# Performance work log

Measured on AMD Instinct MI355X. Metric: run time of the kernel, lower is better.

## Reference

```python
import jax, jax.numpy as jnp
import numpy as np

N, E, C, R = 10000, 160000, 128, 8
D = 4 * C  # 128x0e + 128x1o -> 128*1 + 128*3
INV_SQRT3 = float(1.0 / np.sqrt(3.0))  # CG norm for 1x1->0
INV_SQRT2 = float(1.0 / np.sqrt(2.0))  # CG norm for 1x1->1 (cross)
LIN_SCALE = float(1.0 / np.sqrt(C))    # e3nn Linear fan-in normalization


def _split(x):
    # l-blocked layout: [*, C] scalars then [*, C, 3] vectors
    return x[:, :C], x[:, C:].reshape(x.shape[0], C, 3)


def _merge(f0, f1):
    return jnp.concatenate([f0, f1.reshape(f1.shape[0], 3 * C)], axis=-1)


def _eq_linear(x, W0, W1):
    # equivariant linear: independent channel mixing per l
    f0, f1 = _split(x)
    return _merge((f0 @ W0) * LIN_SCALE, jnp.einsum('eci,cd->edi', f1, W1) * LIN_SCALE)


def _radial_weights(e, Wm1, Wm2, Wm3, Wm4):
    # radial MLP [R]->64->64->64->[5*C]; silu, no bias (e3nn FullyConnectedNet style)
    h = jax.nn.silu(e @ Wm1)
    h = jax.nn.silu(h @ Wm2)
    h = jax.nn.silu(h @ Wm3)
    return (h @ Wm4).reshape(-1, 5, C)  # 5 TP paths x C channels (uvu depthwise)


def setup_inputs() -> dict:
    key = jax.random.key(0)
    k = jax.random.split(key, 14)
    f32 = jnp.float32
    return {
        'node_features': jax.random.normal(k[0], (N, D), f32),
        'edge_features': jax.random.normal(k[1], (E, D), f32),
        'edge_attrs': jax.random.normal(k[2], (E, 4), f32),      # sh l=0 (1) + l=1 (3)
        'edge_embedding': jax.random.normal(k[3], (E, R), f32),  # radial basis
        'sender': jax.random.randint(k[4], (E,), 0, N, jnp.int32),
        'receiver': jax.random.randint(k[5], (E,), 0, N, jnp.int32),
        'Wm1': jax.random.normal(k[6], (R, 64), f32) * float(1.0 / np.sqrt(R)),
        'Wm2': jax.random.normal(k[7], (64, 64), f32) * 0.125,
        'Wm3': jax.random.normal(k[8], (64, 64), f32) * 0.125,
        'Wm4': jax.random.normal(k[9], (64, 5 * C), f32) * 0.125,
        'res_W0': jax.random.normal(k[10], (C, C), f32),
        'res_W1': jax.random.normal(k[11], (C, C), f32),
        'skip_W0': jax.random.normal(k[12], (C, C), f32),
        'skip_W1': jax.random.normal(k[13], (C, C), f32),
    }


def reference(node_features, edge_features, edge_attrs, edge_embedding,
              sender, receiver, Wm1, Wm2, Wm3, Wm4,
              res_W0, res_W1, skip_W0, skip_W1):
    # per-edge radial weights [E, 5, C]
    w = _radial_weights(edge_embedding, Wm1, Wm2, Wm3, Wm4)
    # gather + combine sender/receiver/edge features (all irreps_in)
    comb = node_features[sender] + node_features[receiver] + edge_features
    x0, x1 = _split(comb)                       # [E, C], [E, C, 3]
    sh0, sh1 = edge_attrs[:, 0], edge_attrs[:, 1:4]
    # depthwise (uvu) equivariant tensor product, 5 CG paths
    m0 = (w[:, 0] * x0 * sh0[:, None]
          + w[:, 1] * jnp.einsum('eci,ei->ec', x1, sh1) * INV_SQRT3)
    m1 = (w[:, 2, :, None] * x1 * sh0[:, None, None]
          + w[:, 3, :, None] * x0[:, :, None] * sh1[:, None, :]
          + w[:, 4, :, None] * jnp.cross(x1, sh1[:, None, :]) * INV_SQRT2)
    messages = _merge(m0, m1)                   # [E, D]
    # scatter-add aggregation (fixed num_segments for jit; original uses max+1)
    agg = jax.ops.segment_sum(messages, receiver, num_segments=N)
    out = agg + _eq_linear(agg, res_W0, res_W1)              # residual block
    out = out + _eq_linear(node_features, skip_W0, skip_W1)  # skip connection
    return out
```

## Files before the change

### kernel.cpp

```cpp
#include <hip/hip_runtime.h>

#define NN 10000
#define NE 160000

typedef unsigned short u16;
typedef __bf16 bf16x8 __attribute__((ext_vector_type(8)));
typedef float f32x4 __attribute__((ext_vector_type(4)));

#define INV_SQRT3 0.57735026918962576451f
#define INV_SQRT2 0.70710678118654752440f
#define LIN_SCALE 0.08838834764831845f

#define H3_OFF    0
#define WM4_OFF   20480000
#define WSW_OFF   20561920
#define CNT_OFF   20692992
#define ROFF_OFF  20733952
#define CUR_OFF   20774912
#define EL_OFF    20815872
#define W1F_OFF   21455872
#define W2F_OFF   21459968
#define W3F_OFF   21468160

__device__ __forceinline__ u16 f2bf(float f){
  union { float f; unsigned u; } v; v.f = f;
  unsigned r = v.u + 0x7fffu + ((v.u >> 16) & 1u);
  return (u16)(r >> 16);
}
__device__ __forceinline__ float silu_f(float x){
  return x / (1.f + __expf(-x));
}

union Frag { uint4 u4; bf16x8 bf; };

__global__ __launch_bounds__(256) void prep_weights(
    const float* __restrict__ Wm4, const float* __restrict__ rW0, const float* __restrict__ rW1,
    const float* __restrict__ sW0, const float* __restrict__ sW1,
    const float* __restrict__ Wm1, const float* __restrict__ Wm2, const float* __restrict__ Wm3,
    u16* __restrict__ wm4s, u16* __restrict__ wsw,
    u16* __restrict__ w1f, u16* __restrict__ w2f, u16* __restrict__ w3f,
    int* __restrict__ cnt){
  int t  = blockIdx.x * blockDim.x + threadIdx.x;
  int nt = gridDim.x * blockDim.x;
  if (t < 10240) cnt[t] = 0;
  for (int idx = t; idx < 40960; idx += nt){
    int jj = idx & 7; int lane = (idx >> 3) & 63; int blk = idx >> 9;
    int ks = blk & 1; int ct = blk >> 1;
    int k = ks*32 + ((lane >> 4) << 3) + jj;
    int col = ct*16 + (lane & 15);
    wm4s[idx] = f2bf(Wm4[k*640 + col]);
  }
  for (int idx = t; idx < 2048; idx += nt){
    int jj = idx & 7; int lane = (idx >> 3) & 63; int ct = idx >> 9;
    int k = ((lane >> 4) << 3) + jj;
    int col = ct*16 + (lane & 15);
    w1f[idx] = (k < 8) ? f2bf(Wm1[k*64 + col]) : (u16)0;
  }
  for (int idx = t; idx < 4096; idx += nt){
    int jj = idx & 7; int lane = (idx >> 3) & 63; int blk = idx >> 9;
    int ks = blk & 1; int ct = blk >> 1;
    int k = ks*32 + ((lane >> 4) << 3) + jj;
    int col = ct*16 + (lane & 15);
    w2f[idx] = f2bf(Wm2[k*64 + col]);
    w3f[idx] = f2bf(Wm3[k*64 + col]);
  }
  const float* Ws[4] = { rW0, rW1, sW0, sW1 };
  for (int m = 0; m < 4; ++m){
    const float* src = Ws[m];
    u16* dst = wsw + m*16384;
    for (int idx = t; idx < 16384; idx += nt){
      int jj = idx & 7; int lane = (idx >> 3) & 63; int blk = idx >> 9;
      int ks = blk & 3; int ct = blk >> 2;
      int k = ks*32 + ((lane >> 4) << 3) + jj;
      int col = ct*16 + (lane & 15);
      dst[idx] = f2bf(src[k*128 + col]);
    }
  }
}

__global__ __launch_bounds__(256) void csr_count(const int* __restrict__ rcv, int* __restrict__ cnt){
  int e = blockIdx.x * blockDim.x + threadIdx.x;
  if (e < NE) atomicAdd(&cnt[rcv[e]], 1);
}

__global__ __launch_bounds__(256) void csr_scan(const int* __restrict__ cnt,
                                                int* __restrict__ roff, int* __restrict__ cur){
  __shared__ int s_part[256];
  int t = threadIdx.x;
  int base = t * 40;
  int local = 0;
  for (int i = 0; i < 40; ++i){
    int idx = base + i;
    local += (idx < NN) ? cnt[idx] : 0;
  }
  s_part[t] = local;
  __syncthreads();
  for (int d = 1; d < 256; d <<= 1){
    int v = (t >= d) ? s_part[t - d] : 0;
    __syncthreads();
    s_part[t] += v;
    __syncthreads();
  }
  int run = (t == 0) ? 0 : s_part[t - 1];
  for (int i = 0; i < 40; ++i){
    int idx = base + i;
    if (idx < NN){
      roff[idx] = run;
      cur[idx]  = run;
      run += cnt[idx];
    }
  }
  if (t == 0) roff[NN] = NE;
}

__global__ __launch_bounds__(256) void csr_scatter(const int* __restrict__ rcv,
                                                   int* __restrict__ cur, int* __restrict__ elist){
  int e = blockIdx.x * blockDim.x + threadIdx.x;
  if (e < NE){
    int r = rcv[e];
    int p = atomicAdd(&cur[r], 1);
    elist[p] = e;
  }
}

__global__ __launch_bounds__(256) void zero_agg(float* __restrict__ agg){
  int t = blockIdx.x * blockDim.x + threadIdx.x;
  f32x4* p = (f32x4*)agg;
  const int n4 = NN*512/4;
  for (int i = t; i < n4; i += gridDim.x * blockDim.x){
    f32x4 z = {0.f,0.f,0.f,0.f}; p[i] = z;
  }
}

__global__ __launch_bounds__(256) void radial_mfma_kernel(
    const float* __restrict__ emb, const int* __restrict__ elist,
    const u16* __restrict__ w1f, const u16* __restrict__ w2f, const u16* __restrict__ w3f,
    u16* __restrict__ h3f){
  __shared__ u16 s_w1[2048];
  __shared__ u16 s_w2[4096];
  __shared__ u16 s_w3[4096];
  __shared__ u16 s_h[4][16*72];
  int t = threadIdx.x;
  int lane = t & 63, wave = t >> 6;
  for (int i = t; i < 256; i += 256) ((uint4*)s_w1)[i] = ((const uint4*)w1f)[i];
  for (int i = t; i < 512; i += 256) ((uint4*)s_w2)[i] = ((const uint4*)w2f)[i];
  for (int i = t; i < 512; i += 256) ((uint4*)s_w3)[i] = ((const uint4*)w3f)[i];
  __syncthreads();
  int tid = blockIdx.x*4 + wave;
  int l15 = lane & 15, q = lane >> 4;
  u16* sh = s_h[wave];
  Frag a;
  a.u4.x = 0; a.u4.y = 0; a.u4.z = 0; a.u4.w = 0;
  if (q == 0){
    int eid = elist[tid*16 + l15];
    const float* er = emb + (size_t)eid*8;
    float4 v0 = *(const float4*)er;
    float4 v1 = *(const float4*)(er + 4);
    union { u16 s[8]; uint4 v; } pk;
    pk.s[0]=f2bf(v0.x); pk.s[1]=f2bf(v0.y); pk.s[2]=f2bf(v0.z); pk.s[3]=f2bf(v0.w);
    pk.s[4]=f2bf(v1.x); pk.s[5]=f2bf(v1.y); pk.s[6]=f2bf(v1.z); pk.s[7]=f2bf(v1.w);
    a.u4 = pk.v;
  }
  #pragma unroll
  for (int ct = 0; ct < 4; ++ct){
    Frag b; b.u4 = ((const uint4*)s_w1)[ct*64 + lane];
    f32x4 acc = {0.f,0.f,0.f,0.f};
    acc = __builtin_amdgcn_mfma_f32_16x16x32_bf16(a.bf, b.bf, acc, 0, 0, 0);
    #pragma unroll
    for (int r = 0; r < 4; ++r)
      sh[(q*4 + r)*72 + ct*16 + l15] = f2bf(silu_f(acc[r]));
  }
  asm volatile("s_waitcnt lgkmcnt(0)" ::: "memory");
  __builtin_amdgcn_sched_barrier(0);
  Frag a0, a1;
  a0.u4 = *(const uint4*)(sh + l15*72 + q*8);
  a1.u4 = *(const uint4*)(sh + l15*72 + q*8 + 32);
  float h2[4][4];
  #pragma unroll
  for (int ct = 0; ct < 4; ++ct){
    Frag b0, b1;
    b0.u4 = ((const uint4*)s_w2)[(ct*2 + 0)*64 + lane];
    b1.u4 = ((const uint4*)s_w2)[(ct*2 + 1)*64 + lane];
    f32x4 acc = {0.f,0.f,0.f,0.f};
    acc = __builtin_amdgcn_mfma_f32_16x16x32_bf16(a0.bf, b0.bf, acc, 0, 0, 0);
    acc = __builtin_amdgcn_mfma_f32_16x16x32_bf16(a1.bf, b1.bf, acc, 0, 0, 0);
    #pragma unroll
    for (int r = 0; r < 4; ++r) h2[ct][r] = silu_f(acc[r]);
  }
  #pragma unroll
  for (int ct = 0; ct < 4; ++ct)
    #pragma unroll
    for (int r = 0; r < 4; ++r)
      sh[(q*4 + r)*72 + ct*16 + l15] = f2bf(h2[ct][r]);
  asm volatile("s_waitcnt lgkmcnt(0)" ::: "memory");
  __builtin_amdgcn_sched_barrier(0);
  a0.u4 = *(const uint4*)(sh + l15*72 + q*8);
  a1.u4 = *(const uint4*)(sh + l15*72 + q*8 + 32);
  float h3v[4][4];
  #pragma unroll
  for (int ct = 0; ct < 4; ++ct){
    Frag b0, b1;
    b0.u4 = ((const uint4*)s_w3)[(ct*2 + 0)*64 + lane];
    b1.u4 = ((const uint4*)s_w3)[(ct*2 + 1)*64 + lane];
    f32x4 acc = {0.f,0.f,0.f,0.f};
    acc = __builtin_amdgcn_mfma_f32_16x16x32_bf16(a0.bf, b0.bf, acc, 0, 0, 0);
    acc = __builtin_amdgcn_mfma_f32_16x16x32_bf16(a1.bf, b1.bf, acc, 0, 0, 0);
    #pragma unroll
    for (int r = 0; r < 4; ++r) h3v[ct][r] = silu_f(acc[r]);
  }
  #pragma unroll
  for (int ct = 0; ct < 4; ++ct)
    #pragma unroll
    for (int r = 0; r < 4; ++r)
      sh[(q*4 + r)*72 + ct*16 + l15] = f2bf(h3v[ct][r]);
  asm volatile("s_waitcnt lgkmcnt(0)" ::: "memory");
  __builtin_amdgcn_sched_barrier(0);
  Frag o0, o1;
  o0.u4 = *(const uint4*)(sh + l15*72 + q*8);
  o1.u4 = *(const uint4*)(sh + l15*72 + q*8 + 32);
  uint4* dst = (uint4*)(h3f + (size_t)tid*1024 + lane*16);
  dst[0] = o0.u4;
  dst[1] = o1.u4;
}

__global__ __launch_bounds__(256) void edge_msg_kernel(
    const float* __restrict__ nf, const float* __restrict__ ef, const float* __restrict__ attrs,
    const int* __restrict__ snd, const int* __restrict__ rcv,
    const u16* __restrict__ h3f, const u16* __restrict__ wm4s,
    const int* __restrict__ elist, float* __restrict__ agg){
  __shared__ float s_w[16*650];
  __shared__ int s_eid[16];
  __shared__ int s_rcv[16];
  int t = threadIdx.x;
  int lane = t & 63, wave = t >> 6;
  int e0 = blockIdx.x << 4;
  if (t < 16){
    int eg = elist[e0 + t];
    s_eid[t] = eg;
    s_rcv[t] = rcv[eg];
  }
  Frag a0f, a1f;
  const u16* hp = h3f + (size_t)blockIdx.x*1024 + (size_t)lane*16;
  a0f.u4 = *(const uint4*)(hp);
  a1f.u4 = *(const uint4*)(hp + 8);
  int colb = lane & 15;
  int rowb = (lane >> 4) << 2;
  #pragma unroll
  for (int i = 0; i < 10; ++i){
    int ct = wave*10 + i;
    const u16* bp = wm4s + ((size_t)ct*128 + lane)*8;
    Frag b0f, b1f;
    b0f.u4 = *(const uint4*)(bp);
    b1f.u4 = *(const uint4*)(bp + 512);
    f32x4 acc = {0.f,0.f,0.f,0.f};
    acc = __builtin_amdgcn_mfma_f32_16x16x32_bf16(a0f.bf, b0f.bf, acc, 0, 0, 0);
    acc = __builtin_amdgcn_mfma_f32_16x16x32_bf16(a1f.bf, b1f.bf, acc, 0, 0, 0);
    int cb = ct*16 + colb;
    #pragma unroll
    for (int r = 0; r < 4; ++r) s_w[(rowb + r)*650 + cb] = acc[r];
  }
  __syncthreads();
  int er = t >> 4, l16 = t & 15;
  int eg = s_eid[er];
  int si = snd[eg], ri = s_rcv[er];
  float4 at = *(const float4*)(attrs + (size_t)eg*4);
  float sh0 = at.x, s1x = at.y, s1y = at.z, s1z = at.w;
  const float* ps = nf + (size_t)si*512;
  const float* pr = nf + (size_t)ri*512;
  const float* pe = ef + (size_t)eg*512;
  const float* wr = s_w + er*650;
  float m0[8], m1x[8], m1y[8], m1z[8];
  #pragma unroll
  for (int j = 0; j < 8; ++j){
    int c = j*16 + l16;
    float x0 = ps[c] + pr[c] + pe[c];
    int vb = 128 + 3*c;
    float xa = ps[vb]   + pr[vb]   + pe[vb];
    float xv = ps[vb+1] + pr[vb+1] + pe[vb+1];
    float xc = ps[vb+2] + pr[vb+2] + pe[vb+2];
    float w0 = wr[c], w1 = wr[128 + c], w2 = wr[256 + c], w3 = wr[384 + c], w4 = wr[512 + c];
    float dot = xa*s1x + xv*s1y + xc*s1z;
    m0[j] = w0*x0*sh0 + w1*dot*INV_SQRT3;
    float cr0 = xv*s1z - xc*s1y;
    float cr1 = xc*s1x - xa*s1z;
    float cr2 = xa*s1y - xv*s1x;
    m1x[j] = w2*xa*sh0 + w3*x0*s1x + w4*cr0*INV_SQRT2;
    m1y[j] = w2*xv*sh0 + w3*x0*s1y + w4*cr1*INV_SQRT2;
    m1z[j] = w2*xc*sh0 + w3*x0*s1z + w4*cr2*INV_SQRT2;
  }
  __syncthreads();
  float* mr = s_w + er*520;
  #pragma unroll
  for (int j = 0; j < 8; ++j){
    int c = j*16 + l16;
    int vb = 128 + 3*c;
    mr[c]      = m0[j];
    mr[vb]     = m1x[j];
    mr[vb + 1] = m1y[j];
    mr[vb + 2] = m1z[j];
  }
  __syncthreads();
  float sum0 = 0.f, sum1 = 0.f;
  #pragma unroll
  for (int r = 0; r < 16; ++r){
    sum0 += s_w[r*520 + t];
    sum1 += s_w[r*520 + t + 256];
    if (r == 15 || s_rcv[r] != s_rcv[r + 1]){
      float* ar = agg + (size_t)s_rcv[r]*512;
      unsafeAtomicAdd(ar + t,       sum0);
      unsafeAtomicAdd(ar + t + 256, sum1);
      sum0 = 0.f; sum1 = 0.f;
    }
  }
}

__global__ __launch_bounds__(256) void out_kernel(
    const float* __restrict__ nf, const u16* __restrict__ wsw, float* __restrict__ out){
  __shared__ u16 s_a0[16*136];
  __shared__ u16 s_a1[3][16*136];
  __shared__ u16 s_n0[16*136];
  __shared__ u16 s_n1[3][16*136];
  int t = threadIdx.x;
  int lane = t & 63, wave = t >> 6;
  int n0b = blockIdx.x << 4;
  int nr = t >> 4, l16 = t & 15;
  int node = n0b + nr;
  const float* arow = out + (size_t)node*512;
  const float* nrow = nf  + (size_t)node*512;
  #pragma unroll
  for (int jj = 0; jj < 8; ++jj){
    int c = l16 + jj*16;
    s_a0[nr*136 + c] = f2bf(arow[c]);
    s_n0[nr*136 + c] = f2bf(nrow[c]);
    #pragma unroll
    for (int i = 0; i < 3; ++i){
      s_a1[i][nr*136 + c] = f2bf(arow[128 + 3*c + i]);
      s_n1[i][nr*136 + c] = f2bf(nrow[128 + 3*c + i]);
    }
  }
  __syncthreads();
  int m15 = lane & 15, quad = lane >> 4;
  int aoff = m15*136 + (quad << 3);
  #pragma unroll
  for (int i8 = 0; i8 < 8; ++i8){
    int tt = wave*8 + i8;
    const u16 *Ag, *An, *Bg, *Bn;
    int dt, vi = 0;
    bool scalar = (tt < 8);
    if (scalar){ dt = tt; Ag = s_a0; An = s_n0; Bg = wsw; Bn = wsw + 2*16384; }
    else { vi = (tt - 8) >> 3; dt = (tt - 8) & 7; Ag = s_a1[vi]; An = s_n1[vi]; Bg = wsw + 16384; Bn = wsw + 3*16384; }
    f32x4 acc = {0.f,0.f,0.f,0.f};
    #pragma unroll
    for (int ks = 0; ks < 4; ++ks){
      Frag a, b;
      a.u4 = *(const uint4*)(Ag + aoff + ks*32);
      b.u4 = *(const uint4*)(Bg + ((size_t)(dt*4 + ks)*64 + lane)*8);
      acc = __builtin_amdgcn_mfma_f32_16x16x32_bf16(a.bf, b.bf, acc, 0, 0, 0);
    }
    #pragma unroll
    for (int ks = 0; ks < 4; ++ks){
      Frag a, b;
      a.u4 = *(const uint4*)(An + aoff + ks*32);
      b.u4 = *(const uint4*)(Bn + ((size_t)(dt*4 + ks)*64 + lane)*8);
      acc = __builtin_amdgcn_mfma_f32_16x16x32_bf16(a.bf, b.bf, acc, 0, 0, 0);
    }
    int d = dt*16 + m15;
    int idx = scalar ? d : (128 + 3*d + vi);
    #pragma unroll
    for (int r = 0; r < 4; ++r){
      int nd = n0b + quad*4 + r;
      float val = acc[r]*LIN_SCALE + out[(size_t)nd*512 + idx];
      out[(size_t)nd*512 + idx] = val;
    }
  }
}

extern "C" void kernel_launch(void* const* d_in, const int* in_sizes, int n_in,
                              void* d_out, int out_size, void* d_ws, size_t ws_size,
                              hipStream_t stream){
  (void)in_sizes; (void)n_in; (void)out_size; (void)ws_size;
  const float* nf    = (const float*)d_in[0];
  const float* ef    = (const float*)d_in[1];
  const float* attrs = (const float*)d_in[2];
  const float* emb   = (const float*)d_in[3];
  const int* snd     = (const int*)d_in[4];
  const int* rcv     = (const int*)d_in[5];
  const float* Wm1   = (const float*)d_in[6];
  const float* Wm2   = (const float*)d_in[7];
  const float* Wm3   = (const float*)d_in[8];
  const float* Wm4   = (const float*)d_in[9];
  const float* rW0   = (const float*)d_in[10];
  const float* rW1   = (const float*)d_in[11];
  const float* sW0   = (const float*)d_in[12];
  const float* sW1   = (const float*)d_in[13];
  char* ws  = (char*)d_ws;
  u16* h3f   = (u16*)(ws + H3_OFF);
  u16* wm4s  = (u16*)(ws + WM4_OFF);
  u16* wsw   = (u16*)(ws + WSW_OFF);
  int* cnt   = (int*)(ws + CNT_OFF);
  int* roff  = (int*)(ws + ROFF_OFF);
  int* cur   = (int*)(ws + CUR_OFF);
  int* elist = (int*)(ws + EL_OFF);
  u16* w1f   = (u16*)(ws + W1F_OFF);
  u16* w2f   = (u16*)(ws + W2F_OFF);
  u16* w3f   = (u16*)(ws + W3F_OFF);
  float* out = (float*)d_out;

  prep_weights<<<dim3(80), dim3(256), 0, stream>>>(Wm4, rW0, rW1, sW0, sW1, Wm1, Wm2, Wm3,
                                                   wm4s, wsw, w1f, w2f, w3f, cnt);
  csr_count<<<dim3((NE + 255)/256), dim3(256), 0, stream>>>(rcv, cnt);
  csr_scan<<<dim3(1), dim3(256), 0, stream>>>(cnt, roff, cur);
  csr_scatter<<<dim3((NE + 255)/256), dim3(256), 0, stream>>>(rcv, cur, elist);
  zero_agg<<<dim3(1280), dim3(256), 0, stream>>>(out);
  radial_mfma_kernel<<<dim3(NE/64), dim3(256), 0, stream>>>(emb, elist, w1f, w2f, w3f, h3f);
  edge_msg_kernel<<<dim3(NE/16), dim3(256), 0, stream>>>(nf, ef, attrs, snd, rcv, h3f, wm4s, elist, out);
  out_kernel<<<dim3(NN/16), dim3(256), 0, stream>>>(nf, wsw, out);
}
```

Before: 634.4 us.

## Vectorize edge feature gathers via LDS, coalesce output writes, fuse zeroing into scatter

The edge message kernel now issues the sender, receiver and edge-feature row loads as coalesced 16-byte vector loads at kernel start, before the MFMA weight computation, so their latency overlaps it. It sums the three rows into a shared-memory buffer that the message math then reads, in place of strided scalar global loads. The output kernel stages its linear results in shared memory and does a coalesced vectorized read-modify-write of the output rows. Zeroing the aggregation buffer moves into the CSR scatter kernel to save a launch. In exchange, both kernels use much more LDS, which may lower occupancy.

```diff
diff --git a/kernel.cpp b/kernel.cpp
--- a/kernel.cpp
+++ b/kernel.cpp
@@ -114,21 +114,19 @@
 }
 
 __global__ __launch_bounds__(256) void csr_scatter(const int* __restrict__ rcv,
-                                                   int* __restrict__ cur, int* __restrict__ elist){
+                                                   int* __restrict__ cur, int* __restrict__ elist,
+                                                   float* __restrict__ agg){
   int e = blockIdx.x * blockDim.x + threadIdx.x;
   if (e < NE){
     int r = rcv[e];
     int p = atomicAdd(&cur[r], 1);
     elist[p] = e;
   }
-}
-
-__global__ __launch_bounds__(256) void zero_agg(float* __restrict__ agg){
-  int t = blockIdx.x * blockDim.x + threadIdx.x;
-  f32x4* p = (f32x4*)agg;
+  f32x4* pz = (f32x4*)agg;
   const int n4 = NN*512/4;
-  for (int i = t; i < n4; i += gridDim.x * blockDim.x){
-    f32x4 z = {0.f,0.f,0.f,0.f}; p[i] = z;
+  int nt = gridDim.x * blockDim.x;
+  for (int i = e; i < n4; i += nt){
+    f32x4 z = {0.f,0.f,0.f,0.f}; pz[i] = z;
   }
 }
 
@@ -229,15 +227,29 @@
     const u16* __restrict__ h3f, const u16* __restrict__ wm4s,
     const int* __restrict__ elist, float* __restrict__ agg){
   __shared__ float s_w[16*650];
+  __shared__ float s_comb[16*524];
   __shared__ int s_eid[16];
   __shared__ int s_rcv[16];
   int t = threadIdx.x;
   int lane = t & 63, wave = t >> 6;
   int e0 = blockIdx.x << 4;
   if (t < 16){
-    int eg = elist[e0 + t];
-    s_eid[t] = eg;
-    s_rcv[t] = rcv[eg];
+    int eg0 = elist[e0 + t];
+    s_eid[t] = eg0;
+    s_rcv[t] = rcv[eg0];
+  }
+  __syncthreads();
+  int er = t >> 4, l16 = t & 15;
+  int eg = s_eid[er];
+  int si = snd[eg], ri = s_rcv[er];
+  const f32x4* p4s = (const f32x4*)(nf + (size_t)si*512);
+  const f32x4* p4r = (const f32x4*)(nf + (size_t)ri*512);
+  const f32x4* p4e = (const f32x4*)(ef + (size_t)eg*512);
+  f32x4 ca[8], cb[8], cc[8];
+  #pragma unroll
+  for (int k = 0; k < 8; ++k){
+    int p = l16 + 16*k;
+    ca[k] = p4s[p]; cb[k] = p4r[p]; cc[k] = p4e[p];
   }
   Frag a0f, a1f;
   const u16* hp = h3f + (size_t)blockIdx.x*1024 + (size_t)lane*16;
@@ -255,29 +267,27 @@
     f32x4 acc = {0.f,0.f,0.f,0.f};
     acc = __builtin_amdgcn_mfma_f32_16x16x32_bf16(a0f.bf, b0f.bf, acc, 0, 0, 0);
     acc = __builtin_amdgcn_mfma_f32_16x16x32_bf16(a1f.bf, b1f.bf, acc, 0, 0, 0);
-    int cb = ct*16 + colb;
-    #pragma unroll
-    for (int r = 0; r < 4; ++r) s_w[(rowb + r)*650 + cb] = acc[r];
-  }
-  __syncthreads();
-  int er = t >> 4, l16 = t & 15;
-  int eg = s_eid[er];
-  int si = snd[eg], ri = s_rcv[er];
+    int cb2 = ct*16 + colb;
+    #pragma unroll
+    for (int r = 0; r < 4; ++r) s_w[(rowb + r)*650 + cb2] = acc[r];
+  }
+  #pragma unroll
+  for (int k = 0; k < 8; ++k){
+    f32x4 s = (ca[k] + cb[k]) + cc[k];
+    *(f32x4*)&s_comb[er*524 + (l16 + 16*k)*4] = s;
+  }
+  __syncthreads();
   float4 at = *(const float4*)(attrs + (size_t)eg*4);
   float sh0 = at.x, s1x = at.y, s1y = at.z, s1z = at.w;
-  const float* ps = nf + (size_t)si*512;
-  const float* pr = nf + (size_t)ri*512;
-  const float* pe = ef + (size_t)eg*512;
   const float* wr = s_w + er*650;
+  const float* cr_ = s_comb + er*524;
   float m0[8], m1x[8], m1y[8], m1z[8];
   #pragma unroll
   for (int j = 0; j < 8; ++j){
     int c = j*16 + l16;
-    float x0 = ps[c] + pr[c] + pe[c];
+    float x0 = cr_[c];
     int vb = 128 + 3*c;
-    float xa = ps[vb]   + pr[vb]   + pe[vb];
-    float xv = ps[vb+1] + pr[vb+1] + pe[vb+1];
-    float xc = ps[vb+2] + pr[vb+2] + pe[vb+2];
+    float xa = cr_[vb], xv = cr_[vb+1], xc = cr_[vb+2];
     float w0 = wr[c], w1 = wr[128 + c], w2 = wr[256 + c], w3 = wr[384 + c], w4 = wr[512 + c];
     float dot = xa*s1x + xv*s1y + xc*s1z;
     m0[j] = w0*x0*sh0 + w1*dot*INV_SQRT3;
@@ -320,6 +330,7 @@
   __shared__ u16 s_a1[3][16*136];
   __shared__ u16 s_n0[16*136];
   __shared__ u16 s_n1[3][16*136];
+  __shared__ float s_acc[16*524];
   int t = threadIdx.x;
   int lane = t & 63, wave = t >> 6;
   int n0b = blockIdx.x << 4;
@@ -367,11 +378,18 @@
     int d = dt*16 + m15;
     int idx = scalar ? d : (128 + 3*d + vi);
     #pragma unroll
-    for (int r = 0; r < 4; ++r){
-      int nd = n0b + quad*4 + r;
-      float val = acc[r]*LIN_SCALE + out[(size_t)nd*512 + idx];
-      out[(size_t)nd*512 + idx] = val;
-    }
+    for (int r = 0; r < 4; ++r)
+      s_acc[(quad*4 + r)*524 + idx] = acc[r]*LIN_SCALE;
+  }
+  __syncthreads();
+  #pragma unroll
+  for (int k = 0; k < 8; ++k){
+    int flat4 = t + 256*k;
+    int nd = flat4 >> 7;
+    int col4 = flat4 & 127;
+    f32x4 v = *(const f32x4*)&s_acc[nd*524 + col4*4];
+    f32x4* po = (f32x4*)(out + (size_t)(n0b + nd)*512) + col4;
+    *po = *po + v;
   }
 }
 
@@ -410,8 +428,7 @@
                                                    wm4s, wsw, w1f, w2f, w3f, cnt);
   csr_count<<<dim3((NE + 255)/256), dim3(256), 0, stream>>>(rcv, cnt);
   csr_scan<<<dim3(1), dim3(256), 0, stream>>>(cnt, roff, cur);
-  csr_scatter<<<dim3((NE + 255)/256), dim3(256), 0, stream>>>(rcv, cur, elist);
-  zero_agg<<<dim3(1280), dim3(256), 0, stream>>>(out);
+  csr_scatter<<<dim3((NE + 255)/256), dim3(256), 0, stream>>>(rcv, cur, elist, out);
   radial_mfma_kernel<<<dim3(NE/64), dim3(256), 0, stream>>>(emb, elist, w1f, w2f, w3f, h3f);
   edge_msg_kernel<<<dim3(NE/16), dim3(256), 0, stream>>>(nf, ef, attrs, snd, rcv, h3f, wm4s, elist, out);
   out_kernel<<<dim3(NN/16), dim3(256), 0, stream>>>(nf, wsw, out);
```

Result: no change. 630.7 us (-0.6%).
